# Kernel optimization log

Hardware: AMD Instinct MI355X
Metric: run time of the kernel (lower is better)

Reference implementation:

```python
import jax, jax.numpy as jnp
import numpy as np

PATCH_LEN = 16
D_MODEL = 512


def setup_inputs() -> dict:
    key = jax.random.key(0)
    k_x, k_w1, k_b1, k_w2, k_b2 = jax.random.split(key, 5)
    x = jax.random.normal(k_x, (8, 32, 512), dtype=jnp.float32)
    # Filter_Generators: Linear(patch_len -> d_model), ReLU, Linear(d_model -> patch_len*d_model), ReLU
    s1 = 1.0 / np.sqrt(PATCH_LEN)
    s2 = 1.0 / np.sqrt(D_MODEL)
    W1 = jax.random.uniform(k_w1, (PATCH_LEN, D_MODEL), jnp.float32, -s1, s1)
    b1 = jax.random.uniform(k_b1, (D_MODEL,), jnp.float32, -s1, s1)
    W2 = jax.random.uniform(k_w2, (D_MODEL, PATCH_LEN * D_MODEL), jnp.float32, -s2, s2)
    b2 = jax.random.uniform(k_b2, (PATCH_LEN * D_MODEL,), jnp.float32, -s2, s2)
    return {"x": x, "W1": W1, "b1": b1, "W2": W2, "b2": b2}


def reference(x, W1, b1, W2, b2):
    B = x.shape[0]
    # reshape to patches: (B, N, patch_len)
    xp = x.reshape(B, -1, PATCH_LEN)
    N = xp.shape[1]
    # dynamic filter generation MLP
    h = jax.nn.relu(jnp.einsum('bnp,pd->bnd', xp, W1) + b1)          # (B,N,D)
    filt = jax.nn.relu(jnp.einsum('bnd,de->bne', h, W2) + b2)        # (B,N,P*D)
    # softmax over the sequence (N) axis, per channel (dim=-2 in torch)
    filt = jax.nn.softmax(filt, axis=1)
    filt = filt.reshape(B, N, D_MODEL, PATCH_LEN)                    # (B,N,D,P)
    # broadcast multiply with input patches
    out = filt * xp[:, :, None, :]                                   # (B,N,D,P)
    out = out.transpose(0, 1, 3, 2).reshape(B, N * PATCH_LEN, D_MODEL)
    # AvgPool1d(kernel=3, stride=1, padding=1, count_include_pad=True) over last dim
    p = jnp.pad(out, ((0, 0), (0, 0), (1, 1)))
    out = (p[..., :-2] + p[..., 1:-1] + p[..., 2:]) * (1.0 / 3.0)
    return out
```

## Files before the change

### kernel.cpp

```cpp
#include <hip/hip_runtime.h>
#include <stdint.h>

typedef __attribute__((ext_vector_type(8))) short short8;
typedef __attribute__((ext_vector_type(4))) float floatx4;
typedef unsigned short ushort_t;

__device__ __forceinline__ ushort_t f2bf(float f) {
    union { float f; unsigned int i; } v; v.f = f;
    unsigned int r = v.i + 0x7fffu + ((v.i >> 16) & 1u);
    return (ushort_t)(r >> 16);
}


__global__ __launch_bounds__(256) void k_prep(
    const float* __restrict__ W2, ushort_t* __restrict__ W2T)
{
    __shared__ float t[32][33];
    const int tid = threadIdx.x;
    const int tx = tid & 31, ty = tid >> 5;
    const int e0 = blockIdx.x * 32, k0 = blockIdx.y * 32;
#pragma unroll
    for (int i = 0; i < 4; ++i)
        t[ty + i * 8][tx] = W2[(size_t)(k0 + ty + i * 8) * 8192 + e0 + tx];
    __syncthreads();
#pragma unroll
    for (int i = 0; i < 4; ++i)
        W2T[(size_t)(e0 + ty + i * 8) * 512 + k0 + tx] = f2bf(t[tx][ty + i * 8]);
}

__global__ __launch_bounds__(256) void k1_hidden(
    const float* __restrict__ x, const float* __restrict__ W1,
    const float* __restrict__ b1, ushort_t* __restrict__ h)
{
    __shared__ float xs[16];
    const int r = blockIdx.x;
    const int tid = threadIdx.x;
    if (tid < 16) xs[tid] = x[r * 16 + tid];
    __syncthreads();
#pragma unroll
    for (int dd = 0; dd < 2; ++dd) {
        int d = tid + dd * 256;
        float s = b1[d];
#pragma unroll
        for (int p = 0; p < 16; ++p)
            s += xs[p] * W1[p * 512 + d];
        s = s > 0.f ? s : 0.f;
        h[(size_t)r * 512 + d] = f2bf(s);
    }
}

#define BK 32
__global__ __launch_bounds__(256) void k2_gemm(
    const ushort_t* __restrict__ h,
    const ushort_t* __restrict__ W2T,
    const float* __restrict__ b2,
    float* __restrict__ expws,
    float* __restrict__ denom)
{
    __shared__ __align__(16) ushort_t As[128 * BK];
    __shared__ __align__(16) ushort_t Bs[128 * BK];
    const int tid = threadIdx.x;
    const int lane = tid & 63;
    const int wave = tid >> 6;
    const int quad = lane >> 4;
    const int l16 = lane & 15;
    const int i0 = blockIdx.x * 128;
    const int e0 = blockIdx.y * 128;
    const int wr = (wave >> 1) * 64;
    const int wc = (wave & 1) * 64;

    floatx4 acc[4][4];
#pragma unroll
    for (int i = 0; i < 4; ++i)
#pragma unroll
        for (int j = 0; j < 4; ++j)
            acc[i][j] = (floatx4){0.f, 0.f, 0.f, 0.f};

    for (int k0 = 0; k0 < 512; k0 += BK) {
#pragma unroll
        for (int s = 0; s < 2; ++s) {
            int q = tid + s * 256;
            int row = q >> 2;
            int c = q & 3;
            uint4 va = *reinterpret_cast<const uint4*>(&h[(size_t)(i0 + row) * 512 + k0 + c * 8]);
            uint4 vb = *reinterpret_cast<const uint4*>(&W2T[(size_t)(e0 + row) * 512 + k0 + c * 8]);
            *reinterpret_cast<uint4*>(&As[row * 32 + ((c ^ (row & 3)) << 3)]) = va;
            *reinterpret_cast<uint4*>(&Bs[row * 32 + ((c ^ (row & 3)) << 3)]) = vb;
        }
        __syncthreads();
        short8 af[4], bf[4];
#pragma unroll
        for (int i = 0; i < 4; ++i) {
            int m = wr + i * 16 + l16;
            af[i] = *reinterpret_cast<const short8*>(&As[m * 32 + ((quad ^ (m & 3)) << 3)]);
            int n = wc + i * 16 + l16;
            bf[i] = *reinterpret_cast<const short8*>(&Bs[n * 32 + ((quad ^ (n & 3)) << 3)]);
        }
#pragma unroll
        for (int i = 0; i < 4; ++i)
#pragma unroll
            for (int j = 0; j < 4; ++j)
                acc[i][j] = __builtin_amdgcn_mfma_f32_16x16x32_bf16(af[i], bf[j], acc[i][j], 0, 0, 0);
        __syncthreads();
    }

    const int b_batch = i0 >> 10;
#pragma unroll
    for (int j = 0; j < 4; ++j) {
        int eg = e0 + wc + j * 16 + l16;
        float b2v = b2[eg];
        float csj = 0.f;
#pragma unroll
        for (int i = 0; i < 4; ++i) {
            int rbase = i0 + wr + i * 16 + quad * 4;
#pragma unroll
            for (int r = 0; r < 4; ++r) {
                float v = acc[i][j][r] + b2v;
                v = v > 0.f ? v : 0.f;
                float ev = __expf(v);
                expws[(size_t)(rbase + r) * 8192 + eg] = ev;
                csj += ev;
            }
        }
        csj += __shfl_xor(csj, 16, 64);
        csj += __shfl_xor(csj, 32, 64);
        if (lane < 16) atomicAdd(&denom[b_batch * 8192 + eg], csj);
    }
}

__global__ __launch_bounds__(256) void k_rdenom(const float* __restrict__ denom,
                                                float* __restrict__ rden)
{
    int i = blockIdx.x * 256 + threadIdx.x;
    rden[i] = 1.0f / denom[i];
}

__global__ __launch_bounds__(256) void k3_finalize(
    const float* __restrict__ x,
    const float* __restrict__ rdenom,
    float* __restrict__ out)
{
    __shared__ float xs[16];
    __shared__ float g[16 * 514];
    const int row = blockIdx.x;
    const int b = row >> 10;
    const int tid = threadIdx.x;
    if (tid < 16) xs[tid] = x[row * 16 + tid];
    __syncthreads();
    const float* erow = out + (size_t)row * 8192;
    const float* rd = rdenom + (size_t)b * 8192;
#pragma unroll
    for (int i = 0; i < 8; ++i) {
        int e4 = (tid + i * 256) * 4;
        float4 ev = *reinterpret_cast<const float4*>(erow + e4);
        float4 r4 = *reinterpret_cast<const float4*>(rd + e4);
        int d = e4 >> 4;
        int p0 = e4 & 15;
        g[(p0 + 0) * 514 + d] = ev.x * r4.x * xs[p0 + 0];
        g[(p0 + 1) * 514 + d] = ev.y * r4.y * xs[p0 + 1];
        g[(p0 + 2) * 514 + d] = ev.z * r4.z * xs[p0 + 2];
        g[(p0 + 3) * 514 + d] = ev.w * r4.w * xs[p0 + 3];
    }
    __syncthreads();
    float* orow = out + (size_t)row * 8192;
    const float inv3 = 1.f / 3.f;
#pragma unroll
    for (int i = 0; i < 8; ++i) {
        int flat = tid * 4 + i * 1024;
        int p = flat >> 9;
        int d = flat & 511;
        const float* gr = g + p * 514;
        float gm1 = (d > 0) ? gr[d - 1] : 0.f;
        float g0 = gr[d], g1 = gr[d + 1], g2 = gr[d + 2], g3 = gr[d + 3];
        float g4 = (d < 508) ? gr[d + 4] : 0.f;
        float4 o;
        o.x = (gm1 + g0 + g1) * inv3;
        o.y = (g0 + g1 + g2) * inv3;
        o.z = (g1 + g2 + g3) * inv3;
        o.w = (g2 + g3 + g4) * inv3;
        *reinterpret_cast<float4*>(orow + p * 512 + d) = o;
    }
}

extern "C" void kernel_launch(void* const* d_in, const int* in_sizes, int n_in,
                              void* d_out, int out_size, void* d_ws, size_t ws_size,
                              hipStream_t stream)
{
    const float* x  = (const float*)d_in[0];
    const float* W1 = (const float*)d_in[1];
    const float* b1 = (const float*)d_in[2];
    const float* W2 = (const float*)d_in[3];
    const float* b2 = (const float*)d_in[4];
    float* out = (float*)d_out;

    char* ws = (char*)d_ws;
    ushort_t* h     = (ushort_t*)(ws);
    ushort_t* W2T   = (ushort_t*)(ws + (size_t)(8u << 20));
    float*    denom = (float*)(ws + (size_t)(16u << 20));
    float*    rden  = (float*)(ws + (size_t)(16u << 20) + (256u << 10));

    hipMemsetAsync(denom, 0, 65536 * sizeof(float), stream);
    k_prep<<<dim3(256, 16), 256, 0, stream>>>(W2, W2T);
    k1_hidden<<<8192, 256, 0, stream>>>(x, W1, b1, h);
    k2_gemm<<<dim3(64, 64), 256, 0, stream>>>(h, W2T, b2, out, denom);
    k_rdenom<<<256, 256, 0, stream>>>(denom, rden);
    k3_finalize<<<8192, 256, 0, stream>>>(x, rden, out);
}
```

Baseline: 526.6 us.

## Recompute GEMM in second pass instead of materializing exp filter tensor

Splits the work into two GEMM passes. The first computes only the per-column softmax sums, reduced in shared memory into per-block partials written to the output buffer, which removes the global atomics and the memset. The second recomputes the GEMM with a 16-column halo and fuses the normalization, the multiply by x and the 3-tap average pool directly from registers. This avoids writing and re-reading the 256MB exp intermediate, at the cost of doubling the GEMM FLOPs plus about 25% extra halo columns.

```diff
diff --git a/kernel.cpp b/kernel.cpp
--- a/kernel.cpp
+++ b/kernel.cpp
@@ -49,16 +49,15 @@
     }
 }
 
-#define BK 32
-__global__ __launch_bounds__(256) void k2_gemm(
+__global__ __launch_bounds__(256) void k2_sums(
     const ushort_t* __restrict__ h,
     const ushort_t* __restrict__ W2T,
     const float* __restrict__ b2,
-    float* __restrict__ expws,
-    float* __restrict__ denom)
-{
-    __shared__ __align__(16) ushort_t As[128 * BK];
-    __shared__ __align__(16) ushort_t Bs[128 * BK];
+    float* __restrict__ P)
+{
+    __shared__ __align__(16) ushort_t As[128 * 32];
+    __shared__ __align__(16) ushort_t Bs[128 * 32];
+    __shared__ float csum[128];
     const int tid = threadIdx.x;
     const int lane = tid & 63;
     const int wave = tid >> 6;
@@ -69,6 +68,8 @@
     const int wr = (wave >> 1) * 64;
     const int wc = (wave & 1) * 64;
 
+    if (tid < 128) csum[tid] = 0.f;
+
     floatx4 acc[4][4];
 #pragma unroll
     for (int i = 0; i < 4; ++i)
@@ -76,7 +77,7 @@
         for (int j = 0; j < 4; ++j)
             acc[i][j] = (floatx4){0.f, 0.f, 0.f, 0.f};
 
-    for (int k0 = 0; k0 < 512; k0 += BK) {
+    for (int k0 = 0; k0 < 512; k0 += 32) {
 #pragma unroll
         for (int s = 0; s < 2; ++s) {
             int q = tid + s * 256;
@@ -104,81 +105,157 @@
         __syncthreads();
     }
 
-    const int b_batch = i0 >> 10;
 #pragma unroll
     for (int j = 0; j < 4; ++j) {
         int eg = e0 + wc + j * 16 + l16;
         float b2v = b2[eg];
         float csj = 0.f;
 #pragma unroll
-        for (int i = 0; i < 4; ++i) {
-            int rbase = i0 + wr + i * 16 + quad * 4;
+        for (int i = 0; i < 4; ++i)
 #pragma unroll
             for (int r = 0; r < 4; ++r) {
                 float v = acc[i][j][r] + b2v;
                 v = v > 0.f ? v : 0.f;
-                float ev = __expf(v);
-                expws[(size_t)(rbase + r) * 8192 + eg] = ev;
-                csj += ev;
+                csj += __expf(v);
             }
-        }
         csj += __shfl_xor(csj, 16, 64);
         csj += __shfl_xor(csj, 32, 64);
-        if (lane < 16) atomicAdd(&denom[b_batch * 8192 + eg], csj);
-    }
-}
-
-__global__ __launch_bounds__(256) void k_rdenom(const float* __restrict__ denom,
+        if (lane < 16) atomicAdd(&csum[wc + j * 16 + l16], csj);
+    }
+    __syncthreads();
+    if (tid < 128) P[(size_t)blockIdx.x * 8192 + e0 + tid] = csum[tid];
+}
+
+__global__ __launch_bounds__(256) void k_rdenom(const float* __restrict__ P,
                                                 float* __restrict__ rden)
 {
-    int i = blockIdx.x * 256 + threadIdx.x;
-    rden[i] = 1.0f / denom[i];
-}
-
-__global__ __launch_bounds__(256) void k3_finalize(
+    int idx = blockIdx.x * 256 + threadIdx.x;
+    int b = idx >> 13;
+    int e = idx & 8191;
+    float s = 0.f;
+#pragma unroll
+    for (int j = 0; j < 8; ++j) s += P[(size_t)(b * 8 + j) * 8192 + e];
+    rden[idx] = 1.0f / s;
+}
+
+__global__ __launch_bounds__(256) void k2_final(
+    const ushort_t* __restrict__ h,
+    const ushort_t* __restrict__ W2T,
+    const float* __restrict__ b2,
     const float* __restrict__ x,
-    const float* __restrict__ rdenom,
+    const float* __restrict__ rden,
     float* __restrict__ out)
 {
-    __shared__ float xs[16];
-    __shared__ float g[16 * 514];
-    const int row = blockIdx.x;
-    const int b = row >> 10;
-    const int tid = threadIdx.x;
-    if (tid < 16) xs[tid] = x[row * 16 + tid];
-    __syncthreads();
-    const float* erow = out + (size_t)row * 8192;
-    const float* rd = rdenom + (size_t)b * 8192;
-#pragma unroll
-    for (int i = 0; i < 8; ++i) {
-        int e4 = (tid + i * 256) * 4;
-        float4 ev = *reinterpret_cast<const float4*>(erow + e4);
-        float4 r4 = *reinterpret_cast<const float4*>(rd + e4);
-        int d = e4 >> 4;
-        int p0 = e4 & 15;
-        g[(p0 + 0) * 514 + d] = ev.x * r4.x * xs[p0 + 0];
-        g[(p0 + 1) * 514 + d] = ev.y * r4.y * xs[p0 + 1];
-        g[(p0 + 2) * 514 + d] = ev.z * r4.z * xs[p0 + 2];
-        g[(p0 + 3) * 514 + d] = ev.w * r4.w * xs[p0 + 3];
-    }
-    __syncthreads();
-    float* orow = out + (size_t)row * 8192;
+    __shared__ __align__(16) ushort_t As[128 * 32];
+    __shared__ __align__(16) ushort_t Bs[160 * 32];
+    __shared__ float xs[128 * 17];
+    const int tid = threadIdx.x;
+    const int lane = tid & 63;
+    const int wave = tid >> 6;
+    const int quad = lane >> 4;
+    const int l16 = lane & 15;
+    const int i0 = blockIdx.x * 128;
+    const int d0 = blockIdx.y * 8;
+    const int ebase = blockIdx.y * 128 - 16;
+    const int wrow = wave * 32;
+    const int b = i0 >> 10;
+
+#pragma unroll
+    for (int s = 0; s < 8; ++s) {
+        int q = tid + s * 256;
+        xs[(q >> 4) * 17 + (q & 15)] = x[(size_t)(i0 + (q >> 4)) * 16 + (q & 15)];
+    }
+
+    floatx4 acc[2][10];
+#pragma unroll
+    for (int i = 0; i < 2; ++i)
+#pragma unroll
+        for (int t = 0; t < 10; ++t)
+            acc[i][t] = (floatx4){0.f, 0.f, 0.f, 0.f};
+
+    for (int k0 = 0; k0 < 512; k0 += 32) {
+#pragma unroll
+        for (int s = 0; s < 2; ++s) {
+            int q = tid + s * 256;
+            int row = q >> 2, c = q & 3;
+            uint4 va = *reinterpret_cast<const uint4*>(&h[(size_t)(i0 + row) * 512 + k0 + c * 8]);
+            *reinterpret_cast<uint4*>(&As[row * 32 + ((c ^ (row & 3)) << 3)]) = va;
+        }
+#pragma unroll
+        for (int s = 0; s < 3; ++s) {
+            int q = tid + s * 256;
+            if (q < 640) {
+                int row = q >> 2, c = q & 3;
+                int eg = ebase + row;
+                eg = eg < 0 ? 0 : (eg > 8191 ? 8191 : eg);
+                uint4 vb = *reinterpret_cast<const uint4*>(&W2T[(size_t)eg * 512 + k0 + c * 8]);
+                *reinterpret_cast<uint4*>(&Bs[row * 32 + ((c ^ (row & 3)) << 3)]) = vb;
+            }
+        }
+        __syncthreads();
+        short8 af[2], bf[10];
+#pragma unroll
+        for (int i = 0; i < 2; ++i) {
+            int m = wrow + i * 16 + l16;
+            af[i] = *reinterpret_cast<const short8*>(&As[m * 32 + ((quad ^ (m & 3)) << 3)]);
+        }
+#pragma unroll
+        for (int t = 0; t < 10; ++t) {
+            int n = t * 16 + l16;
+            bf[t] = *reinterpret_cast<const short8*>(&Bs[n * 32 + ((quad ^ (n & 3)) << 3)]);
+        }
+#pragma unroll
+        for (int i = 0; i < 2; ++i)
+#pragma unroll
+            for (int t = 0; t < 10; ++t)
+                acc[i][t] = __builtin_amdgcn_mfma_f32_16x16x32_bf16(af[i], bf[t], acc[i][t], 0, 0, 0);
+        __syncthreads();
+    }
+
+#pragma unroll
+    for (int t = 0; t < 10; ++t) {
+        int el = t * 16 + l16;
+        int eg = ebase + el;
+        int valid = (eg >= 0) & (eg < 8192);
+        int egc = valid ? eg : 0;
+        float b2v = b2[egc];
+        float scale = valid ? rden[b * 8192 + egc] : 0.f;
+#pragma unroll
+        for (int i = 0; i < 2; ++i) {
+            int rbase = wrow + i * 16 + quad * 4;
+#pragma unroll
+            for (int r = 0; r < 4; ++r) {
+                float v = acc[i][t][r] + b2v;
+                v = v > 0.f ? v : 0.f;
+                acc[i][t][r] = __expf(v) * scale * xs[(rbase + r) * 17 + l16];
+            }
+        }
+    }
+
     const float inv3 = 1.f / 3.f;
 #pragma unroll
-    for (int i = 0; i < 8; ++i) {
-        int flat = tid * 4 + i * 1024;
-        int p = flat >> 9;
-        int d = flat & 511;
-        const float* gr = g + p * 514;
-        float gm1 = (d > 0) ? gr[d - 1] : 0.f;
-        float g0 = gr[d], g1 = gr[d + 1], g2 = gr[d + 2], g3 = gr[d + 3];
-        float g4 = (d < 508) ? gr[d + 4] : 0.f;
-        float4 o;
-        o.x = (gm1 + g0 + g1) * inv3;
-        o.y = (g0 + g1 + g2) * inv3;
-        o.z = (g1 + g2 + g3) * inv3;
-        o.w = (g2 + g3 + g4) * inv3;
-        *reinterpret_cast<float4*>(orow + p * 512 + d) = o;
+    for (int i = 0; i < 2; ++i) {
+        int rbase = wrow + i * 16 + quad * 4;
+#pragma unroll
+        for (int r = 0; r < 4; ++r) {
+            int row = rbase + r;
+            float g0 = acc[i][0][r], g1 = acc[i][1][r], g2 = acc[i][2][r];
+            float g3 = acc[i][3][r], g4 = acc[i][4][r], g5 = acc[i][5][r];
+            float g6 = acc[i][6][r], g7 = acc[i][7][r], g8 = acc[i][8][r];
+            float g9 = acc[i][9][r];
+            float4 o1, o2;
+            o1.x = (g0 + g1 + g2) * inv3;
+            o1.y = (g1 + g2 + g3) * inv3;
+            o1.z = (g2 + g3 + g4) * inv3;
+            o1.w = (g3 + g4 + g5) * inv3;
+            o2.x = (g4 + g5 + g6) * inv3;
+            o2.y = (g5 + g6 + g7) * inv3;
+            o2.z = (g6 + g7 + g8) * inv3;
+            o2.w = (g7 + g8 + g9) * inv3;
+            size_t orow = (size_t)((i0 + row) * 16 + l16);
+            *reinterpret_cast<float4*>(&out[orow * 512 + d0]) = o1;
+            *reinterpret_cast<float4*>(&out[orow * 512 + d0 + 4]) = o2;
+        }
     }
 }
 
@@ -194,15 +271,14 @@
     float* out = (float*)d_out;
 
     char* ws = (char*)d_ws;
-    ushort_t* h     = (ushort_t*)(ws);
-    ushort_t* W2T   = (ushort_t*)(ws + (size_t)(8u << 20));
-    float*    denom = (float*)(ws + (size_t)(16u << 20));
-    float*    rden  = (float*)(ws + (size_t)(16u << 20) + (256u << 10));
-
-    hipMemsetAsync(denom, 0, 65536 * sizeof(float), stream);
+    ushort_t* h    = (ushort_t*)(ws);
+    ushort_t* W2T  = (ushort_t*)(ws + (size_t)(8u << 20));
+    float*    rden = (float*)(ws + (size_t)(16u << 20));
+    float*    P    = (float*)d_out;
+
     k_prep<<<dim3(256, 16), 256, 0, stream>>>(W2, W2T);
     k1_hidden<<<8192, 256, 0, stream>>>(x, W1, b1, h);
-    k2_gemm<<<dim3(64, 64), 256, 0, stream>>>(h, W2T, b2, out, denom);
-    k_rdenom<<<256, 256, 0, stream>>>(denom, rden);
-    k3_finalize<<<8192, 256, 0, stream>>>(x, rden, out);
-}
+    k2_sums<<<dim3(64, 64), 256, 0, stream>>>(h, W2T, b2, P);
+    k_rdenom<<<256, 256, 0, stream>>>(P, rden);
+    k2_final<<<dim3(64, 64), 256, 0, stream>>>(h, W2T, b2, x, rden, out);
+}
```

Result: slower. 597.5 us (+13.4%).
